# Kernel optimization log

Hardware: AMD Instinct MI355X
Metric: run time of the kernel (lower is better)

Reference implementation:

```python
import jax, jax.numpy as jnp
import numpy as np

BLOCK = 64
EPS = 1e-6
N_HEADS = 16


def _rope(t, cos, sin):
    # t: (B,S,H,hd); cos/sin: (S, hd//2) -> broadcast (1,S,1,hd//2)
    B, S, H, hd = t.shape
    tr = t.reshape(B, S, H, hd // 2, 2)
    t0, t1 = tr[..., 0], tr[..., 1]
    c = cos[None, :, None, :]
    s = sin[None, :, None, :]
    o0 = t0 * c - t1 * s
    o1 = t0 * s + t1 * c
    return jnp.stack([o0, o1], axis=-1).reshape(B, S, H, hd)


def setup_inputs() -> dict:
    key = jax.random.key(0)
    ks = jax.random.split(key, 6)
    B, S, D = 1, 2048, 2048
    hd = D // N_HEADS
    x = jax.random.normal(ks[0], (B, S, D), dtype=jnp.float32)
    # rotary table: theta_i = 10000^(-2i/hd)
    inv_freq = 1.0 / (10000.0 ** (jnp.arange(0, hd, 2, dtype=jnp.float32) / hd))
    t = jnp.arange(S, dtype=jnp.float32)
    freqs = jnp.outer(t, inv_freq)  # (S, hd//2)
    freqs_cos = jnp.cos(freqs)
    freqs_sin = jnp.sin(freqs)
    std = 0.02
    Wq = jax.random.normal(ks[1], (D, D), dtype=jnp.float32) * std
    Wk = jax.random.normal(ks[2], (D, D), dtype=jnp.float32) * std
    Wv = jax.random.normal(ks[3], (D, D), dtype=jnp.float32) * std
    Wo = jax.random.normal(ks[4], (D, D), dtype=jnp.float32) * std
    mask = jnp.ones((1, 1), dtype=bool)  # non-None mask => no masking in original code
    return {"x": x, "freqs_cos": freqs_cos, "freqs_sin": freqs_sin,
            "Wq": Wq, "Wk": Wk, "Wv": Wv, "Wo": Wo, "mask": mask}


def reference(x, freqs_cos, freqs_sin, Wq, Wk, Wv, Wo, mask):
    B, S, D = x.shape
    H = N_HEADS
    hd = D // H
    scale = hd ** -0.5
    nb = S // BLOCK

    q = (x @ Wq.T).reshape(B, S, H, hd)
    k = (x @ Wk.T).reshape(B, S, H, hd)
    v = (x @ Wv.T).reshape(B, S, H, hd)
    q = _rope(q, freqs_cos, freqs_sin)
    k = _rope(k, freqs_cos, freqs_sin)

    # block views: (B, nb, BLOCK, H, hd)
    qb = q.reshape(B, nb, BLOCK, H, hd)
    kb = k.reshape(B, nb, BLOCK, H, hd)
    vb = v.reshape(B, nb, BLOCK, H, hd)

    # per-(i,j) block scores: (B, nb_i, nb_j, H, BLOCK_q, BLOCK_k)
    s = jnp.einsum('binhd,bjmhd->bijhnm', qb, kb) * scale
    # NOTE: original module (mask is not None path) applies NO causal mask and
    # uses the per-block local max (no running-max rescale) -- reproduced exactly.
    m = jnp.max(s, axis=-1, keepdims=True)
    p = jnp.exp(s - m)
    # denominator: sum of per-block row sums over all j blocks -> (B, nb, H, BLOCK)
    L = p.sum(axis=-1).sum(axis=2)
    # numerator: sum over j blocks of p @ v -> (B, nb, BLOCK, H, hd)
    O = jnp.einsum('bijhnm,bjmhd->binhd', p, vb).reshape(B, S, H, hd)
    Lr = L.transpose(0, 1, 3, 2).reshape(B, S, H, 1)  # (B,S,H,1)
    O = O / (Lr + EPS)
    return O.reshape(B, S, D) @ Wo.T
```

## Files before the change

kernel.cpp:

```cpp
#include <hip/hip_runtime.h>
#include <hip/hip_bf16.h>
#include <math.h>

#define SEQ 2048
#define DM  2048
#define NH  16
#define HD  128
#define SCALE 0.08838834764831845f

typedef __bf16 bf16_t;
typedef __bf16 bf16x8 __attribute__((ext_vector_type(8)));
typedef __bf16 bf16x4 __attribute__((ext_vector_type(4)));
typedef float  f32x4  __attribute__((ext_vector_type(4)));
typedef int    i32x4  __attribute__((ext_vector_type(4)));

typedef const __attribute__((address_space(1))) void* gas_ptr;
typedef __attribute__((address_space(3))) void* las_ptr;

__device__ __forceinline__ void gload_lds16(const void* g, void* l) {
    __builtin_amdgcn_global_load_lds((gas_ptr)g, (las_ptr)l, 16, 0, 0);
}

__device__ __forceinline__ f32x4 mfma_bf16(bf16x8 a, bf16x8 b, f32x4 c) {
    return __builtin_amdgcn_mfma_f32_16x16x32_bf16(a, b, c, 0, 0, 0);
}

__device__ __forceinline__ unsigned cvtpk_bf16(float lo, float hi) {
    unsigned d;
    asm("v_cvt_pk_bf16_f32 %0, %1, %2" : "=v"(d) : "v"(lo), "v"(hi));
    return d;
}

__device__ __forceinline__ bf16x8 read_frag64(const bf16_t* lds, int row, int k) {
    int chunk = (k >> 3) ^ (row & 7);
    return *(const bf16x8*)(lds + row * 64 + chunk * 8);
}
__device__ __forceinline__ bf16x8 read_frag128(const bf16_t* lds, int row, int k) {
    int chunk = k >> 3;
    chunk = (chunk & 8) | ((chunk ^ row) & 7);
    return *(const bf16x8*)(lds + row * 128 + chunk * 8);
}
__device__ __forceinline__ bf16x8 read_slab(const bf16_t* sl, int row, int g) {
    int j = g ^ ((row >> 1) & 3);
    return *(const bf16x8*)(sl + row * 32 + j * 8);
}

__global__ __launch_bounds__(256) void cvt5(
    const float* __restrict__ s0, const float* __restrict__ s1,
    const float* __restrict__ s2, const float* __restrict__ s3,
    const float* __restrict__ s4,
    bf16_t* __restrict__ d0, bf16_t* __restrict__ d1, bf16_t* __restrict__ d2,
    bf16_t* __restrict__ d3, bf16_t* __restrict__ d4)
{
    int which = blockIdx.y;
    const float* s; bf16_t* d;
    switch (which) {
        case 0: s = s0; d = d0; break;
        case 1: s = s1; d = d1; break;
        case 2: s = s2; d = d2; break;
        case 3: s = s3; d = d3; break;
        default: s = s4; d = d4; break;
    }
    size_t idx = ((size_t)blockIdx.x * 256 + threadIdx.x) * 4;
    float4 v = *(const float4*)(s + idx);
    bf16x4 o = { (bf16_t)v.x, (bf16_t)v.y, (bf16_t)v.z, (bf16_t)v.w };
    *(bf16x4*)(d + idx) = o;
}

#define BARX() asm volatile("s_barrier" ::: "memory")
#define VMW8 asm volatile("s_waitcnt vmcnt(8)" ::: "memory")
#define VMW4 asm volatile("s_waitcnt vmcnt(4)" ::: "memory")
#define VMW0 asm volatile("s_waitcnt vmcnt(0)" ::: "memory")
#define NOGATE

__global__ __launch_bounds__(512, 2) void qkv_pipe(
    const bf16_t* __restrict__ A,
    const bf16_t* __restrict__ B0, const bf16_t* __restrict__ B1,
    const bf16_t* __restrict__ B2,
    bf16_t* __restrict__ Oq, bf16_t* __restrict__ Ok, bf16_t* __restrict__ Ov,
    const float* __restrict__ fcos, const float* __restrict__ fsin)
{
    __shared__ bf16_t lds[65536];

    const int tid = threadIdx.x;
    const int lane = tid & 63;
    const int w = tid >> 6;
    const int wm = w >> 2;
    const int wn = w & 3;
    const int g4 = lane >> 4, r15 = lane & 15;

    const int bm = blockIdx.y;
    const int bny = blockIdx.x;
    const int sel = bny >> 3;
    const int bnl = bny & 7;
    const bf16_t* Bp = (sel == 0) ? B0 : (sel == 1) ? B1 : B2;

    const size_t arow0 = (size_t)bm * 256;
    const size_t brow0 = (size_t)bnl * 256;

    const int row0 = tid >> 2;
    const int kj0  = (tid & 3) ^ ((row0 >> 1) & 3);
    const bf16_t* pA = A  + (arow0 + row0) * DM + kj0 * 8;
    const bf16_t* pB = Bp + (brow0 + row0) * DM + kj0 * 8;
    char* ldsb = (char*)lds;
    const int off0 = tid * 16;
    const int off1 = 8192 + tid * 16;

    #define STAGE_HT(S) do { if ((S) < 128) {                                   \
        const int T_ = (S) >> 2, a_ = (S) & 3;                                  \
        const int ko_ = T_ * 64 + ((a_ >> 1) << 5);                             \
        char* dst_ = ldsb + (((T_ & 1) << 16) | ((a_ & 1) << 15) | ((a_ >> 1) << 14)); \
        const bf16_t* s0_ = (a_ & 1) ? pB : pA;                                 \
        gload_lds16(s0_ + ko_, dst_ + off0);                                    \
        gload_lds16(s0_ + 128 * DM + ko_, dst_ + off1);                         \
    } } while (0)

    const bf16_t* b0A0 = lds;
    const bf16_t* b0A1 = lds + 8192;
    const bf16_t* b0B0 = lds + 16384;
    const bf16_t* b0B1 = lds + 24576;
    const bf16_t* b1A0 = lds + 32768;
    const bf16_t* b1A1 = lds + 40960;
    const bf16_t* b1B0 = lds + 49152;
    const bf16_t* b1B1 = lds + 57344;

    f32x4 acc[8][4] = {};

    #define PHASE2(ASL, BSL, S1, S2, GATE)                                      \
    {                                                                           \
        GATE;                                                                   \
        _Pragma("unroll")                                                       \
        for (int k = 0; k < 8; ++k)                                             \
            af[k] = read_slab((ASL), wm * 128 + k * 16 + r15, g4);              \
        _Pragma("unroll")                                                       \
        for (int n = 0; n < 4; ++n)                                             \
            bfr[n] = read_slab((BSL), wn * 64 + n * 16 + r15, g4);              \
        STAGE_HT(S1);                                                           \
        STAGE_HT(S2);                                                           \
        BARX();                                                                 \
        __builtin_amdgcn_s_setprio(1);                                          \
        _Pragma("unroll")                                                       \
        for (int k = 0; k < 8; ++k)                                             \
            _Pragma("unroll")                                                   \
            for (int n = 0; n < 4; ++n)                                         \
                acc[k][n] = mfma_bf16(af[k], bfr[n], acc[k][n]);                \
        __builtin_amdgcn_s_setprio(0);                                          \
        BARX();                                                                 \
    }

    STAGE_HT(0); STAGE_HT(1); STAGE_HT(2); STAGE_HT(3); STAGE_HT(4); STAGE_HT(5);
    VMW8;
    BARX();

    for (int i = 0; i < 15; ++i) {
        const int s0 = 6 + i * 8;
        bf16x8 af[8], bfr[4];
        PHASE2(b0A0, b0B0, s0 + 0, s0 + 1, VMW8)
        PHASE2(b0A1, b0B1, s0 + 2, s0 + 3, VMW8)
        PHASE2(b1A0, b1B0, s0 + 4, s0 + 5, VMW8)
        PHASE2(b1A1, b1B1, s0 + 6, s0 + 7, VMW8)
    }
    {
        bf16x8 af[8], bfr[4];
        PHASE2(b0A0, b0B0, 126, 127, VMW8)
        PHASE2(b0A1, b0B1, 200, 200, VMW8)
        PHASE2(b1A0, b1B0, 200, 200, VMW4)
        PHASE2(b1A1, b1B1, 200, 200, VMW0)
    }
    #undef PHASE2
    #undef STAGE_HT

    const int r0 = bm * 256 + wm * 128;
    const int c0 = bnl * 256 + wn * 64;

    if (sel == 2) {
        #pragma unroll
        for (int m = 0; m < 8; ++m) {
            int rowb = r0 + m * 16 + g4 * 4;
            #pragma unroll
            for (int n = 0; n < 4; ++n) {
                int col = c0 + n * 16 + r15;
                bf16x4 pk = { (bf16_t)acc[m][n][0], (bf16_t)acc[m][n][1],
                              (bf16_t)acc[m][n][2], (bf16_t)acc[m][n][3] };
                *(bf16x4*)&Ov[(size_t)col * SEQ + rowb] = pk;
            }
        }
    } else {
        bf16_t* dst = (sel == 0) ? Oq : Ok;
        #pragma unroll
        for (int m = 0; m < 8; ++m) {
            int rowb = r0 + m * 16 + g4 * 4;
            #pragma unroll
            for (int n = 0; n < 4; ++n) {
                int col = c0 + n * 16 + r15;
                int f = (col & (HD - 1)) >> 1;
                float sgn = (col & 1) ? 1.0f : -1.0f;
                #pragma unroll
                for (int r = 0; r < 4; ++r) {
                    float mine = acc[m][n][r];
                    float other = __shfl_xor(mine, 1);
                    float cc = fcos[(rowb + r) * (HD / 2) + f];
                    float ss = fsin[(rowb + r) * (HD / 2) + f];
                    float o = mine * cc + sgn * other * ss;
                    dst[(size_t)(rowb + r) * DM + col] = (bf16_t)o;
                }
            }
        }
    }
}

__global__ __launch_bounds__(256) void gemm_fin(
    const bf16_t* __restrict__ A, const bf16_t* __restrict__ B0,
    float* __restrict__ Of)
{
    __shared__ bf16_t lA[128 * 64];
    __shared__ bf16_t lB[64 * 64];

    const int tid = threadIdx.x;
    const int lane = tid & 63;
    const int w = tid >> 6;
    const int wm = w >> 1, wn = w & 1;
    const int g = lane >> 4, r15 = lane & 15;

    const int bm = blockIdx.x;
    const int bn = blockIdx.y;

    f32x4 acc[4][2] = {};

    const size_t arow0 = (size_t)bm * 128;
    const size_t brow0 = (size_t)bn * 64;

    for (int kt = 0; kt < DM / 64; ++kt) {
        const int k0 = kt * 64;
        #pragma unroll
        for (int i = 0; i < 4; ++i) {
            int c = i * 256 + tid;
            int row = c >> 3;
            int ck = (c ^ row) & 7;
            const bf16_t* ga = A + (arow0 + row) * DM + k0 + ck * 8;
            gload_lds16(ga, (char*)lA + (i * 256 + w * 64) * 16);
        }
        #pragma unroll
        for (int i = 0; i < 2; ++i) {
            int c = i * 256 + tid;
            int row = c >> 3;
            int ck = (c ^ row) & 7;
            const bf16_t* gb = B0 + (brow0 + row) * DM + k0 + ck * 8;
            gload_lds16(gb, (char*)lB + (i * 256 + w * 64) * 16);
        }
        __syncthreads();
        #pragma unroll
        for (int kk = 0; kk < 2; ++kk) {
            bf16x8 af[4], bfr[2];
            #pragma unroll
            for (int m = 0; m < 4; ++m)
                af[m] = read_frag64(lA, wm * 64 + m * 16 + r15, kk * 32 + g * 8);
            #pragma unroll
            for (int n = 0; n < 2; ++n)
                bfr[n] = read_frag64(lB, wn * 32 + n * 16 + r15, kk * 32 + g * 8);
            #pragma unroll
            for (int m = 0; m < 4; ++m)
                #pragma unroll
                for (int n = 0; n < 2; ++n)
                    acc[m][n] = mfma_bf16(af[m], bfr[n], acc[m][n]);
        }
        __syncthreads();
    }

    const int r0 = bm * 128 + wm * 64;
    const int c0 = bn * 64 + wn * 32;
    #pragma unroll
    for (int m = 0; m < 4; ++m) {
        int rowb = r0 + m * 16 + g * 4;
        #pragma unroll
        for (int n = 0; n < 2; ++n) {
            int col = c0 + n * 16 + r15;
            #pragma unroll
            for (int r = 0; r < 4; ++r)
                Of[(size_t)(rowb + r) * DM + col] = acc[m][n][r];
        }
    }
}

__global__ __launch_bounds__(256, 2) void attn_k6(
    const bf16_t* __restrict__ Q, const bf16_t* __restrict__ Kb,
    const bf16_t* __restrict__ Vt, bf16_t* __restrict__ Op,
    float* __restrict__ Lp)
{
    __shared__ bf16_t lk[2 * 64 * 128];
    __shared__ bf16_t lv[2 * 128 * 64];

    const int tid = threadIdx.x;
    const int lane = tid & 63;
    const int w = tid >> 6;
    const int g = lane >> 4, r15 = lane & 15;
    const int qb = blockIdx.x;
    const int h = blockIdx.y;
    const int sp = blockIdx.z;
    const int j0 = sp * 16;

    const int lo = g & 1, hb = g >> 1;
    const int e_src = (lo << 5) + r15;
    const int o_src = e_src + 16;
    const int sA = hb ? o_src : e_src;
    const int sB = hb ? e_src : o_src;

    bf16x8 qf[2][4];
    #pragma unroll
    for (int u = 0; u < 2; ++u) {
        const bf16_t* qrow = Q + (size_t)(qb * 128 + w * 32 + u * 16 + r15) * DM + h * HD + g * 8;
        #pragma unroll
        for (int ks = 0; ks < 4; ++ks)
            qf[u][ks] = *(const bf16x8*)(qrow + ks * 32);
    }

    f32x4 oacc[2][8] = {};
    float Lsum[2] = {0.f, 0.f};

    #define STAGE_KV(JJ, BUF)                                                     \
    {                                                                             \
        _Pragma("unroll")                                                         \
        for (int i = 0; i < 4; ++i) {                                             \
            int c = i * 256 + tid;                                                \
            int row = c >> 4, ckl = c & 15;                                       \
            int ck = (ckl & 8) | ((ckl ^ row) & 7);                               \
            const bf16_t* gk = Kb + (size_t)((JJ) * 64 + row) * DM + h * HD + ck * 8; \
            gload_lds16(gk, (char*)lk + (BUF) * 16384 + (i * 256 + w * 64) * 16); \
        }                                                                         \
        _Pragma("unroll")                                                         \
        for (int i = 0; i < 4; ++i) {                                             \
            int c = i * 256 + tid;                                                \
            int row = c >> 3;                                                     \
            int ck = (c ^ row) & 7;                                               \
            const bf16_t* gv = Vt + (size_t)(h * HD + row) * SEQ + (JJ) * 64 + ck * 8; \
            gload_lds16(gv, (char*)lv + (BUF) * 16384 + (i * 256 + w * 64) * 16); \
        }                                                                         \
    }

    STAGE_KV(j0, 0);
    asm volatile("s_waitcnt vmcnt(0)" ::: "memory");
    __builtin_amdgcn_s_barrier();

    for (int jj = 0; jj < 16; ++jj) {
        const int cur = jj & 1;
        const bf16_t* lkc = lk + cur * 8192;
        const bf16_t* lvc = lv + cur * 8192;
        if (jj < 15) STAGE_KV(j0 + jj + 1, cur ^ 1);

        f32x4 sacc[2][4] = {};
        __builtin_amdgcn_s_setprio(1);
        #pragma unroll
        for (int ks = 0; ks < 4; ++ks) {
            #pragma unroll
            for (int n = 0; n < 4; ++n) {
                bf16x8 kf = read_frag128(lkc, n * 16 + r15, ks * 32 + g * 8);
                sacc[0][n] = mfma_bf16(kf, qf[0][ks], sacc[0][n]);
                sacc[1][n] = mfma_bf16(kf, qf[1][ks], sacc[1][n]);
            }
        }
        __builtin_amdgcn_s_setprio(0);

        bf16x8 pa0[2], pa1[2];
        #pragma unroll
        for (int u = 0; u < 2; ++u) {
            float mx0 = fmaxf(fmaxf(sacc[u][0][0], sacc[u][0][1]), fmaxf(sacc[u][0][2], sacc[u][0][3]));
            float mx1 = fmaxf(fmaxf(sacc[u][1][0], sacc[u][1][1]), fmaxf(sacc[u][1][2], sacc[u][1][3]));
            float mx2 = fmaxf(fmaxf(sacc[u][2][0], sacc[u][2][1]), fmaxf(sacc[u][2][2], sacc[u][2][3]));
            float mx3 = fmaxf(fmaxf(sacc[u][3][0], sacc[u][3][1]), fmaxf(sacc[u][3][2], sacc[u][3][3]));
            float mx = fmaxf(fmaxf(mx0, mx1), fmaxf(mx2, mx3));
            mx = fmaxf(mx, __shfl_xor(mx, 16));
            mx = fmaxf(mx, __shfl_xor(mx, 32));

            float p[4][4];
            float ls = 0.f;
            #pragma unroll
            for (int n = 0; n < 4; ++n)
                #pragma unroll
                for (int r = 0; r < 4; ++r) {
                    float pv = __expf((sacc[u][n][r] - mx) * SCALE);
                    p[n][r] = pv;
                    ls += pv;
                }
            Lsum[u] += ls;

            unsigned D00 = cvtpk_bf16(p[0][0], p[0][1]), D01 = cvtpk_bf16(p[0][2], p[0][3]);
            unsigned D10 = cvtpk_bf16(p[1][0], p[1][1]), D11 = cvtpk_bf16(p[1][2], p[1][3]);
            unsigned D20 = cvtpk_bf16(p[2][0], p[2][1]), D21 = cvtpk_bf16(p[2][2], p[2][3]);
            unsigned D30 = cvtpk_bf16(p[3][0], p[3][1]), D31 = cvtpk_bf16(p[3][2], p[3][3]);

            unsigned r0 = __shfl((int)(lo ? D10 : D00), sA);
            unsigned r1 = __shfl((int)(lo ? D11 : D01), sA);
            unsigned r2 = __shfl((int)(lo ? D00 : D10), sB);
            unsigned r3 = __shfl((int)(lo ? D01 : D11), sB);
            unsigned r4 = __shfl((int)(lo ? D30 : D20), sA);
            unsigned r5 = __shfl((int)(lo ? D31 : D21), sA);
            unsigned r6 = __shfl((int)(lo ? D20 : D30), sB);
            unsigned r7 = __shfl((int)(lo ? D21 : D31), sB);
            i32x4 w0, w1;
            w0[0] = (int)(hb ? r2 : r0);  w0[1] = (int)(hb ? r3 : r1);
            w0[2] = (int)(hb ? r0 : r2);  w0[3] = (int)(hb ? r1 : r3);
            w1[0] = (int)(hb ? r6 : r4);  w1[1] = (int)(hb ? r7 : r5);
            w1[2] = (int)(hb ? r4 : r6);  w1[3] = (int)(hb ? r5 : r7);
            pa0[u] = __builtin_bit_cast(bf16x8, w0);
            pa1[u] = __builtin_bit_cast(bf16x8, w1);
        }

        __builtin_amdgcn_s_setprio(1);
        #pragma unroll
        for (int n = 0; n < 8; ++n) {
            bf16x8 bv0 = read_frag64(lvc, n * 16 + r15, g * 8);
            oacc[0][n] = mfma_bf16(pa0[0], bv0, oacc[0][n]);
            oacc[1][n] = mfma_bf16(pa0[1], bv0, oacc[1][n]);
            bf16x8 bv1 = read_frag64(lvc, n * 16 + r15, 32 + g * 8);
            oacc[0][n] = mfma_bf16(pa1[0], bv1, oacc[0][n]);
            oacc[1][n] = mfma_bf16(pa1[1], bv1, oacc[1][n]);
        }
        __builtin_amdgcn_s_setprio(0);

        asm volatile("s_waitcnt vmcnt(0)" ::: "memory");
        __builtin_amdgcn_s_barrier();
    }

    #pragma unroll
    for (int u = 0; u < 2; ++u) {
        float L = Lsum[u];
        L += __shfl_xor(L, 16);
        L += __shfl_xor(L, 32);
        int qrow = qb * 128 + w * 32 + u * 16;
        if (g == 0)
            Lp[((size_t)sp * NH + h) * SEQ + qrow + r15] = L;

        #pragma unroll
        for (int n = 0; n < 8; ++n) {
            int col = h * HD + n * 16 + r15;
            int rowb = qrow + g * 4;
            #pragma unroll
            for (int r = 0; r < 4; ++r)
                Op[(size_t)sp * SEQ * DM + (size_t)(rowb + r) * DM + col] = (bf16_t)oacc[u][n][r];
        }
    }
}

__global__ __launch_bounds__(256) void attn_cmb(
    const bf16_t* __restrict__ Op, const float* __restrict__ Lp,
    bf16_t* __restrict__ Ob)
{
    const int row = blockIdx.x;
    const int c0 = threadIdx.x * 8;
    const int h = c0 >> 7;

    float L = 1e-6f;
    #pragma unroll
    for (int s = 0; s < 2; ++s)
        L += Lp[((size_t)s * NH + h) * SEQ + row];

    float acc[8] = {};
    #pragma unroll
    for (int s = 0; s < 2; ++s) {
        bf16x8 v = *(const bf16x8*)(Op + (size_t)s * SEQ * DM + (size_t)row * DM + c0);
        #pragma unroll
        for (int j = 0; j < 8; ++j)
            acc[j] += (float)v[j];
    }
    float inv = 1.0f / L;
    bf16x8 o;
    #pragma unroll
    for (int j = 0; j < 8; ++j)
        o[j] = (bf16_t)(acc[j] * inv);
    *(bf16x8*)(Ob + (size_t)row * DM + c0) = o;
}

extern "C" void kernel_launch(void* const* d_in, const int* in_sizes, int n_in,
                              void* d_out, int out_size, void* d_ws, size_t ws_size,
                              hipStream_t stream)
{
    const float* x    = (const float*)d_in[0];
    const float* fcos = (const float*)d_in[1];
    const float* fsin = (const float*)d_in[2];
    const float* Wq   = (const float*)d_in[3];
    const float* Wk   = (const float*)d_in[4];
    const float* Wv   = (const float*)d_in[5];
    const float* Wo   = (const float*)d_in[6];
    float* out = (float*)d_out;

    const size_t NE = (size_t)DM * SEQ;
    bf16_t* ws  = (bf16_t*)d_ws;
    bf16_t* xb  = ws;
    bf16_t* wqb = ws + 1 * NE;
    bf16_t* wkb = ws + 2 * NE;
    bf16_t* wvb = ws + 3 * NE;
    bf16_t* wob = ws + 4 * NE;
    bf16_t* qr  = ws + 5 * NE;
    bf16_t* kr  = ws + 6 * NE;
    bf16_t* vt  = ws + 7 * NE;
    bf16_t* ob  = ws + 8 * NE;
    bf16_t* op  = ws;
    float*  lp  = (float*)(ws + 9 * NE);

    hipLaunchKernelGGL(cvt5, dim3(4096, 5), dim3(256), 0, stream,
                       x, Wq, Wk, Wv, Wo, xb, wqb, wkb, wvb, wob);

    hipLaunchKernelGGL(qkv_pipe, dim3(24, 8), dim3(512), 0, stream,
                       xb, wqb, wkb, wvb, qr, kr, vt, fcos, fsin);

    hipLaunchKernelGGL(attn_k6, dim3(16, 16, 2), dim3(256), 0, stream,
                       qr, kr, vt, op, lp);

    hipLaunchKernelGGL(attn_cmb, dim3(2048), dim3(256), 0, stream,
                       op, lp, ob);

    hipLaunchKernelGGL(gemm_fin, dim3(16, 32), dim3(256), 0, stream,
                       ob, wob, out);
}
```

Measured before the change: 166.1 us.

## Fuse attention split-combine and Wo conversion into output projection GEMM

Removes the attn_cmb kernel and the Wo fp32->bf16 conversion pass. The final GEMM now reads both partial attention outputs, normalizes them by the summed denominators, converts fp32 Wo tiles on the fly, and writes the results to LDS with ordinary stores. This saves two kernel launches and an intermediate round-trip through global memory. In exchange it drops the async global_load_lds path, performs redundant normalization work across the 32 column blocks, and reads Wo in fp32 from every row block.

```diff
diff --git a/kernel.cpp b/kernel.cpp
--- a/kernel.cpp
+++ b/kernel.cpp
@@ -210,8 +210,8 @@
 }
 
 __global__ __launch_bounds__(256) void gemm_fin(
-    const bf16_t* __restrict__ A, const bf16_t* __restrict__ B0,
-    float* __restrict__ Of)
+    const bf16_t* __restrict__ Op, const float* __restrict__ Lp,
+    const float* __restrict__ Wo, float* __restrict__ Of)
 {
     __shared__ bf16_t lA[128 * 64];
     __shared__ bf16_t lB[64 * 64];
@@ -227,8 +227,8 @@
 
     f32x4 acc[4][2] = {};
 
-    const size_t arow0 = (size_t)bm * 128;
-    const size_t brow0 = (size_t)bn * 64;
+    const int arow0 = bm * 128;
+    const int brow0 = bn * 64;
 
     for (int kt = 0; kt < DM / 64; ++kt) {
         const int k0 = kt * 64;
@@ -237,16 +237,30 @@
             int c = i * 256 + tid;
             int row = c >> 3;
             int ck = (c ^ row) & 7;
-            const bf16_t* ga = A + (arow0 + row) * DM + k0 + ck * 8;
-            gload_lds16(ga, (char*)lA + (i * 256 + w * 64) * 16);
+            int gr = arow0 + row;
+            int gc = k0 + ck * 8;
+            int h = gc >> 7;
+            float L = Lp[(size_t)h * SEQ + gr] + Lp[(size_t)(NH + h) * SEQ + gr] + 1e-6f;
+            float inv = 1.0f / L;
+            bf16x8 v0 = *(const bf16x8*)(Op + (size_t)gr * DM + gc);
+            bf16x8 v1 = *(const bf16x8*)(Op + (size_t)SEQ * DM + (size_t)gr * DM + gc);
+            bf16x8 o;
+            #pragma unroll
+            for (int j = 0; j < 8; ++j)
+                o[j] = (bf16_t)(((float)v0[j] + (float)v1[j]) * inv);
+            *(bf16x8*)((char*)lA + c * 16) = o;
         }
         #pragma unroll
         for (int i = 0; i < 2; ++i) {
             int c = i * 256 + tid;
             int row = c >> 3;
             int ck = (c ^ row) & 7;
-            const bf16_t* gb = B0 + (brow0 + row) * DM + k0 + ck * 8;
-            gload_lds16(gb, (char*)lB + (i * 256 + w * 64) * 16);
+            const float* src = Wo + (size_t)(brow0 + row) * DM + k0 + ck * 8;
+            float4 f0 = *(const float4*)(src);
+            float4 f1 = *(const float4*)(src + 4);
+            bf16x8 o = { (bf16_t)f0.x, (bf16_t)f0.y, (bf16_t)f0.z, (bf16_t)f0.w,
+                         (bf16_t)f1.x, (bf16_t)f1.y, (bf16_t)f1.z, (bf16_t)f1.w };
+            *(bf16x8*)((char*)lB + c * 16) = o;
         }
         __syncthreads();
         #pragma unroll
@@ -441,35 +455,6 @@
     }
 }
 
-__global__ __launch_bounds__(256) void attn_cmb(
-    const bf16_t* __restrict__ Op, const float* __restrict__ Lp,
-    bf16_t* __restrict__ Ob)
-{
-    const int row = blockIdx.x;
-    const int c0 = threadIdx.x * 8;
-    const int h = c0 >> 7;
-
-    float L = 1e-6f;
-    #pragma unroll
-    for (int s = 0; s < 2; ++s)
-        L += Lp[((size_t)s * NH + h) * SEQ + row];
-
-    float acc[8] = {};
-    #pragma unroll
-    for (int s = 0; s < 2; ++s) {
-        bf16x8 v = *(const bf16x8*)(Op + (size_t)s * SEQ * DM + (size_t)row * DM + c0);
-        #pragma unroll
-        for (int j = 0; j < 8; ++j)
-            acc[j] += (float)v[j];
-    }
-    float inv = 1.0f / L;
-    bf16x8 o;
-    #pragma unroll
-    for (int j = 0; j < 8; ++j)
-        o[j] = (bf16_t)(acc[j] * inv);
-    *(bf16x8*)(Ob + (size_t)row * DM + c0) = o;
-}
-
 extern "C" void kernel_launch(void* const* d_in, const int* in_sizes, int n_in,
                               void* d_out, int out_size, void* d_ws, size_t ws_size,
                               hipStream_t stream)
@@ -489,16 +474,15 @@
     bf16_t* wqb = ws + 1 * NE;
     bf16_t* wkb = ws + 2 * NE;
     bf16_t* wvb = ws + 3 * NE;
-    bf16_t* wob = ws + 4 * NE;
     bf16_t* qr  = ws + 5 * NE;
     bf16_t* kr  = ws + 6 * NE;
     bf16_t* vt  = ws + 7 * NE;
-    bf16_t* ob  = ws + 8 * NE;
     bf16_t* op  = ws;
     float*  lp  = (float*)(ws + 9 * NE);
 
-    hipLaunchKernelGGL(cvt5, dim3(4096, 5), dim3(256), 0, stream,
-                       x, Wq, Wk, Wv, Wo, xb, wqb, wkb, wvb, wob);
+    hipLaunchKernelGGL(cvt5, dim3(4096, 4), dim3(256), 0, stream,
+                       x, Wq, Wk, Wv, (const float*)nullptr,
+                       xb, wqb, wkb, wvb, (bf16_t*)nullptr);
 
     hipLaunchKernelGGL(qkv_pipe, dim3(24, 8), dim3(512), 0, stream,
                        xb, wqb, wkb, wvb, qr, kr, vt, fcos, fsin);
@@ -506,9 +490,6 @@
     hipLaunchKernelGGL(attn_k6, dim3(16, 16, 2), dim3(256), 0, stream,
                        qr, kr, vt, op, lp);
 
-    hipLaunchKernelGGL(attn_cmb, dim3(2048), dim3(256), 0, stream,
-                       op, lp, ob);
-
     hipLaunchKernelGGL(gemm_fin, dim3(16, 32), dim3(256), 0, stream,
-                       ob, wob, out);
-}
+                       op, lp, Wo, out);
+}
```

Result: slower. 276.5 us (+66.4%).

## Replace pipelined 256x256 QKV GEMM with simple 128x128 single-buffered tiles

Applied to the files above, without the earlier changes.

Replaces the QKV projection kernel, which used 256x256 tiles, 512 threads, double-buffered LDS and hand-scheduled waitcnt pipelining, with a plain 128x128-tile kernel. The new kernel has 256 threads, a K step of 32 and one LDS buffer guarded by __syncthreads. The grid grows from 192 to 768 blocks, and the three weight matrices are addressed through one contiguous base pointer, relying on wq/wk/wv being adjacent in the workspace. This aims for better occupancy and CU coverage. It gives up the load/compute overlap and the operand reuse of the larger tiles, and adds two barriers per 32-wide K step.

```diff
diff --git a/kernel.cpp b/kernel.cpp
--- a/kernel.cpp
+++ b/kernel.cpp
@@ -67,134 +67,88 @@
     *(bf16x4*)(d + idx) = o;
 }
 
-#define BARX() asm volatile("s_barrier" ::: "memory")
-#define VMW8 asm volatile("s_waitcnt vmcnt(8)" ::: "memory")
-#define VMW4 asm volatile("s_waitcnt vmcnt(4)" ::: "memory")
-#define VMW0 asm volatile("s_waitcnt vmcnt(0)" ::: "memory")
-#define NOGATE
-
-__global__ __launch_bounds__(512, 2) void qkv_pipe(
-    const bf16_t* __restrict__ A,
-    const bf16_t* __restrict__ B0, const bf16_t* __restrict__ B1,
-    const bf16_t* __restrict__ B2,
+__global__ __launch_bounds__(256, 3) void qkv_m97(
+    const bf16_t* __restrict__ A, const bf16_t* __restrict__ Ball,
     bf16_t* __restrict__ Oq, bf16_t* __restrict__ Ok, bf16_t* __restrict__ Ov,
     const float* __restrict__ fcos, const float* __restrict__ fsin)
 {
-    __shared__ bf16_t lds[65536];
+    __shared__ bf16_t lA[128 * 32];
+    __shared__ bf16_t lB[128 * 32];
 
     const int tid = threadIdx.x;
     const int lane = tid & 63;
     const int w = tid >> 6;
-    const int wm = w >> 2;
-    const int wn = w & 3;
+    const int wm = w >> 1, wn = w & 1;
     const int g4 = lane >> 4, r15 = lane & 15;
 
+    const int bn = blockIdx.x;
     const int bm = blockIdx.y;
-    const int bny = blockIdx.x;
-    const int sel = bny >> 3;
-    const int bnl = bny & 7;
-    const bf16_t* Bp = (sel == 0) ? B0 : (sel == 1) ? B1 : B2;
-
-    const size_t arow0 = (size_t)bm * 256;
-    const size_t brow0 = (size_t)bnl * 256;
-
-    const int row0 = tid >> 2;
-    const int kj0  = (tid & 3) ^ ((row0 >> 1) & 3);
-    const bf16_t* pA = A  + (arow0 + row0) * DM + kj0 * 8;
-    const bf16_t* pB = Bp + (brow0 + row0) * DM + kj0 * 8;
-    char* ldsb = (char*)lds;
-    const int off0 = tid * 16;
-    const int off1 = 8192 + tid * 16;
-
-    #define STAGE_HT(S) do { if ((S) < 128) {                                   \
-        const int T_ = (S) >> 2, a_ = (S) & 3;                                  \
-        const int ko_ = T_ * 64 + ((a_ >> 1) << 5);                             \
-        char* dst_ = ldsb + (((T_ & 1) << 16) | ((a_ & 1) << 15) | ((a_ >> 1) << 14)); \
-        const bf16_t* s0_ = (a_ & 1) ? pB : pA;                                 \
-        gload_lds16(s0_ + ko_, dst_ + off0);                                    \
-        gload_lds16(s0_ + 128 * DM + ko_, dst_ + off1);                         \
-    } } while (0)
-
-    const bf16_t* b0A0 = lds;
-    const bf16_t* b0A1 = lds + 8192;
-    const bf16_t* b0B0 = lds + 16384;
-    const bf16_t* b0B1 = lds + 24576;
-    const bf16_t* b1A0 = lds + 32768;
-    const bf16_t* b1A1 = lds + 40960;
-    const bf16_t* b1B0 = lds + 49152;
-    const bf16_t* b1B1 = lds + 57344;
-
-    f32x4 acc[8][4] = {};
-
-    #define PHASE2(ASL, BSL, S1, S2, GATE)                                      \
-    {                                                                           \
-        GATE;                                                                   \
-        _Pragma("unroll")                                                       \
-        for (int k = 0; k < 8; ++k)                                             \
-            af[k] = read_slab((ASL), wm * 128 + k * 16 + r15, g4);              \
-        _Pragma("unroll")                                                       \
-        for (int n = 0; n < 4; ++n)                                             \
-            bfr[n] = read_slab((BSL), wn * 64 + n * 16 + r15, g4);              \
-        STAGE_HT(S1);                                                           \
-        STAGE_HT(S2);                                                           \
-        BARX();                                                                 \
-        __builtin_amdgcn_s_setprio(1);                                          \
-        _Pragma("unroll")                                                       \
-        for (int k = 0; k < 8; ++k)                                             \
-            _Pragma("unroll")                                                   \
-            for (int n = 0; n < 4; ++n)                                         \
-                acc[k][n] = mfma_bf16(af[k], bfr[n], acc[k][n]);                \
-        __builtin_amdgcn_s_setprio(0);                                          \
-        BARX();                                                                 \
-    }
-
-    STAGE_HT(0); STAGE_HT(1); STAGE_HT(2); STAGE_HT(3); STAGE_HT(4); STAGE_HT(5);
-    VMW8;
-    BARX();
-
-    for (int i = 0; i < 15; ++i) {
-        const int s0 = 6 + i * 8;
-        bf16x8 af[8], bfr[4];
-        PHASE2(b0A0, b0B0, s0 + 0, s0 + 1, VMW8)
-        PHASE2(b0A1, b0B1, s0 + 2, s0 + 3, VMW8)
-        PHASE2(b1A0, b1B0, s0 + 4, s0 + 5, VMW8)
-        PHASE2(b1A1, b1B1, s0 + 6, s0 + 7, VMW8)
-    }
-    {
-        bf16x8 af[8], bfr[4];
-        PHASE2(b0A0, b0B0, 126, 127, VMW8)
-        PHASE2(b0A1, b0B1, 200, 200, VMW8)
-        PHASE2(b1A0, b1B0, 200, 200, VMW4)
-        PHASE2(b1A1, b1B1, 200, 200, VMW0)
-    }
-    #undef PHASE2
-    #undef STAGE_HT
-
-    const int r0 = bm * 256 + wm * 128;
-    const int c0 = bnl * 256 + wn * 64;
+    const int sel = bn >> 4;
+
+    const size_t arow0 = (size_t)bm * 128;
+    const size_t brow0 = (size_t)bn * 128;
+
+    const int rw0 = tid >> 2,        kj0 = (tid & 3) ^ ((rw0 >> 1) & 3);
+    const int rw1 = (256 + tid) >> 2, kj1 = ((256 + tid) & 3) ^ ((rw1 >> 1) & 3);
+    const bf16_t* pA0 = A    + (arow0 + rw0) * DM + kj0 * 8;
+    const bf16_t* pA1 = A    + (arow0 + rw1) * DM + kj1 * 8;
+    const bf16_t* pB0 = Ball + (brow0 + rw0) * DM + kj0 * 8;
+    const bf16_t* pB1 = Ball + (brow0 + rw1) * DM + kj1 * 8;
+    char* dA0 = (char*)lA + tid * 16;
+    char* dA1 = (char*)lA + (256 + tid) * 16;
+    char* dB0 = (char*)lB + tid * 16;
+    char* dB1 = (char*)lB + (256 + tid) * 16;
+
+    f32x4 acc[4][4] = {};
+
+    for (int kt = 0; kt < DM / 32; ++kt) {
+        const int k0 = kt * 32;
+        gload_lds16(pA0 + k0, dA0);
+        gload_lds16(pA1 + k0, dA1);
+        gload_lds16(pB0 + k0, dB0);
+        gload_lds16(pB1 + k0, dB1);
+        __syncthreads();
+
+        bf16x8 af[4], bfr[4];
+        #pragma unroll
+        for (int m = 0; m < 4; ++m)
+            af[m] = read_slab(lA, wm * 64 + m * 16 + r15, g4);
+        #pragma unroll
+        for (int n = 0; n < 4; ++n)
+            bfr[n] = read_slab(lB, wn * 64 + n * 16 + r15, g4);
+        #pragma unroll
+        for (int m = 0; m < 4; ++m)
+            #pragma unroll
+            for (int n = 0; n < 4; ++n)
+                acc[m][n] = mfma_bf16(af[m], bfr[n], acc[m][n]);
+        __syncthreads();
+    }
+
+    const int r0 = bm * 128 + wm * 64;
+    const int c0g = bn * 128 + wn * 64;
 
     if (sel == 2) {
         #pragma unroll
-        for (int m = 0; m < 8; ++m) {
+        for (int m = 0; m < 4; ++m) {
             int rowb = r0 + m * 16 + g4 * 4;
             #pragma unroll
             for (int n = 0; n < 4; ++n) {
-                int col = c0 + n * 16 + r15;
+                int colr = (c0g + n * 16 + r15) & 2047;
                 bf16x4 pk = { (bf16_t)acc[m][n][0], (bf16_t)acc[m][n][1],
                               (bf16_t)acc[m][n][2], (bf16_t)acc[m][n][3] };
-                *(bf16x4*)&Ov[(size_t)col * SEQ + rowb] = pk;
+                *(bf16x4*)&Ov[(size_t)colr * SEQ + rowb] = pk;
             }
         }
     } else {
         bf16_t* dst = (sel == 0) ? Oq : Ok;
         #pragma unroll
-        for (int m = 0; m < 8; ++m) {
+        for (int m = 0; m < 4; ++m) {
             int rowb = r0 + m * 16 + g4 * 4;
             #pragma unroll
             for (int n = 0; n < 4; ++n) {
-                int col = c0 + n * 16 + r15;
-                int f = (col & (HD - 1)) >> 1;
-                float sgn = (col & 1) ? 1.0f : -1.0f;
+                int colr = (c0g + n * 16 + r15) & 2047;
+                int f = (colr & (HD - 1)) >> 1;
+                float sgn = (colr & 1) ? 1.0f : -1.0f;
                 #pragma unroll
                 for (int r = 0; r < 4; ++r) {
                     float mine = acc[m][n][r];
@@ -202,7 +156,7 @@
                     float cc = fcos[(rowb + r) * (HD / 2) + f];
                     float ss = fsin[(rowb + r) * (HD / 2) + f];
                     float o = mine * cc + sgn * other * ss;
-                    dst[(size_t)(rowb + r) * DM + col] = (bf16_t)o;
+                    dst[(size_t)(rowb + r) * DM + colr] = (bf16_t)o;
                 }
             }
         }
@@ -500,8 +454,8 @@
     hipLaunchKernelGGL(cvt5, dim3(4096, 5), dim3(256), 0, stream,
                        x, Wq, Wk, Wv, Wo, xb, wqb, wkb, wvb, wob);
 
-    hipLaunchKernelGGL(qkv_pipe, dim3(24, 8), dim3(512), 0, stream,
-                       xb, wqb, wkb, wvb, qr, kr, vt, fcos, fsin);
+    hipLaunchKernelGGL(qkv_m97, dim3(48, 16), dim3(256), 0, stream,
+                       xb, wqb, qr, kr, vt, fcos, fsin);
 
     hipLaunchKernelGGL(attn_k6, dim3(16, 16, 2), dim3(256), 0, stream,
                        qr, kr, vt, op, lp);
```

Result: slower. 170.0 us (+2.3%).
